# Kernel optimization log

Measured on AMD Instinct MI355X. Metric: run time of the kernel, lower is better.

## Reference

```python
import jax, jax.numpy as jnp
import numpy as np

VOCAB, D_EMB, H, M, B, L = 50000, 512, 512, 512, 1024, 64


def _lstm_last_h(x, seqlen, kernel, bias):
    """Run BasicLSTMCell over time; return hidden state at t=seqlen (TF dynamic_rnn semantics).
    x: [B, L, D], seqlen: [B], kernel: [D+H, 4H] (i,j,f,o), bias: [4H]."""
    Bc, Lc, _ = x.shape
    xT = jnp.swapaxes(x, 0, 1)  # [L, B, D]

    def step(carry, inp):
        c, h = carry
        xt, t = inp
        gates = jnp.concatenate([xt, h], axis=-1) @ kernel + bias
        i, j, f, o = jnp.split(gates, 4, axis=-1)
        new_c = c * jax.nn.sigmoid(f + 1.0) + jax.nn.sigmoid(i) * jnp.tanh(j)
        new_h = jnp.tanh(new_c) * jax.nn.sigmoid(o)
        mask = (t < seqlen)[:, None]
        return (jnp.where(mask, new_c, c), jnp.where(mask, new_h, h)), None

    z = jnp.zeros((Bc, kernel.shape[1] // 4), x.dtype)
    (c, h), _ = jax.lax.scan(step, (z, z), (xT, jnp.arange(Lc)))
    return h


def _reverse_seq(x, seqlen):
    """tf.reverse_sequence: reverse first seqlen steps per row, keep padding in place."""
    Bc, Lc, _ = x.shape
    t = jnp.arange(Lc)[None, :]
    idx = jnp.where(t < seqlen[:, None], seqlen[:, None] - 1 - t, t)
    return jnp.take_along_axis(x, idx[:, :, None], axis=1)


def _encode(x, seqlen, k_fw, b_fw, k_bw, b_bw):
    h_fw = _lstm_last_h(x, seqlen, k_fw, b_fw)
    h_bw = _lstm_last_h(_reverse_seq(x, seqlen), seqlen, k_bw, b_bw)
    return jnp.concatenate([h_fw, h_bw], axis=1)  # [B, 2H]


def setup_inputs() -> dict:
    key = jax.random.key(0)
    ks = jax.random.split(key, 12)
    s_emb = 1.0 / np.sqrt(D_EMB)
    s_k = 1.0 / np.sqrt(D_EMB + H)
    return {
        "input1": jax.random.randint(ks[0], (B, L), 0, VOCAB, dtype=jnp.int32),
        "input2": jax.random.randint(ks[1], (B, L), 0, VOCAB, dtype=jnp.int32),
        "seqlen1": jax.random.randint(ks[2], (B,), 1, L + 1, dtype=jnp.int32),
        "seqlen2": jax.random.randint(ks[3], (B,), 1, L + 1, dtype=jnp.int32),
        "embedding": jax.random.normal(ks[4], (VOCAB, D_EMB), jnp.float32) * s_emb,
        "k_fw": jax.random.normal(ks[5], (D_EMB + H, 4 * H), jnp.float32) * s_k,
        "b_fw": jnp.zeros((4 * H,), jnp.float32),
        "k_bw": jax.random.normal(ks[6], (D_EMB + H, 4 * H), jnp.float32) * s_k,
        "b_bw": jnp.zeros((4 * H,), jnp.float32),
        "W1": jax.random.normal(ks[7], (3 * 2 * H + 1, M), jnp.float32) / np.sqrt(6 * H + 1),
        "b1": jax.random.normal(ks[8], (1, M), jnp.float32) * 0.01,
        "W2": jax.random.normal(ks[9], (M, 2), jnp.float32) / np.sqrt(M),
        "b2": jax.random.normal(ks[10], (1, 2), jnp.float32) * 0.01,
    }


def reference(input1, input2, seqlen1, seqlen2, embedding, k_fw, b_fw, k_bw, b_bw, W1, b1, W2, b2):
    x1 = embedding[input1]  # [B, L, D]
    x2 = embedding[input2]
    h1 = _encode(x1, seqlen1, k_fw, b_fw, k_bw, b_bw)  # [B, 2H]
    h2 = _encode(x2, seqlen2, k_fw, b_fw, k_bw, b_bw)
    h_dist = jnp.sum(jnp.square(h1 - h2), axis=1, keepdims=True)  # [B, 1]
    h_combined = jnp.concatenate([h1, h2, h_dist, h1 * h2], axis=1)  # [B, 6H+1]
    e1 = jax.nn.relu(h_combined @ W1 + b1)  # dropout keep_prob=1 at inference
    preds = e1 @ W2 + b2  # [B, 2]
    return preds
```

## Files before the change

kernel.cpp:

```cpp
#include <hip/hip_runtime.h>
#include <hip/hip_bf16.h>
#include <cstddef>

#define VOCAB 50000
#define D_EMB 512
#define HDIM  512
#define MDIM  512
#define BATCH 1024
#define SEQL  64
#define ROWS  2048
#define KTOT  1024
#define HC_K  3136

typedef _Float16 f16;
typedef __attribute__((ext_vector_type(8))) _Float16 f16x8;
typedef __attribute__((ext_vector_type(4))) float f32x4;

__device__ __forceinline__ float sigf(float x) {
    return 1.0f / (1.0f + __expf(-x));
}
__device__ __forceinline__ float tanh_fast(float x) {
    x = fminf(30.0f, fmaxf(-30.0f, x));
    float t = __expf(-2.0f * x);
    return (1.0f - t) / (1.0f + t);
}
__device__ __forceinline__ void glds16(const void* g, const void* lds) {
    __builtin_amdgcn_global_load_lds(
        (const __attribute__((address_space(1))) unsigned int*)g,
        (__attribute__((address_space(3))) unsigned int*)lds, 16, 0, 0);
}

__global__ __launch_bounds__(256) void conv_emb(const float* __restrict__ src,
                                                f16* __restrict__ dst, int n8) {
    int i = blockIdx.x * 256 + threadIdx.x;
    if (i >= n8) return;
    const float4* s = (const float4*)src + (size_t)i * 2;
    float4 a = s[0], b = s[1];
    f16x8 o = {(f16)a.x, (f16)a.y, (f16)a.z, (f16)a.w,
               (f16)b.x, (f16)b.y, (f16)b.z, (f16)b.w};
    *(f16x8*)&dst[(size_t)i * 8] = o;
}

__global__ __launch_bounds__(256) void pack_w(const float* __restrict__ kfw,
                                              const float* __restrict__ kbw,
                                              f16* __restrict__ Wt) {
    unsigned idx = blockIdx.x * 256 + threadIdx.x;
    int k    = idx & 1023;
    int colp = (idx >> 10) & 2047;
    int d    = idx >> 21;
    int cg = colp >> 6, g = (colp >> 4) & 3, ci = colp & 15;
    int n = cg * 16 + ci;
    const float* K = d ? kbw : kfw;
    Wt[idx] = (f16)K[(size_t)k * 2048 + g * 512 + n];
}

__global__ __launch_bounds__(256) void pack_w1(const float* __restrict__ W1,
                                               f16* __restrict__ W1t) {
    int idx = blockIdx.x * 256 + threadIdx.x;
    if (idx >= 512 * HC_K) return;
    int k = idx % HC_K, c = idx / HC_K;
    W1t[idx] = (k < 3073) ? (f16)W1[(size_t)k * MDIM + c] : (f16)0.0f;
}

__global__ __launch_bounds__(256, 2) void lstm_step(
    int t,
    const int* __restrict__ in1, const int* __restrict__ in2,
    const int* __restrict__ sl1, const int* __restrict__ sl2,
    const f16* __restrict__ embH,
    const f16* __restrict__ Wt,
    const float* __restrict__ bfw, const float* __restrict__ bbw,
    const f16* __restrict__ hin,
    f16* __restrict__ hout,
    float* __restrict__ cbuf)
{
    const int dir = blockIdx.z;
    const int bx  = blockIdx.x;
    const int by  = blockIdx.y;
    const int tid = threadIdx.x;
    const int l = tid & 63, w = tid >> 6;

    __shared__ f16 Atile[2][128 * 64];
    __shared__ f16 Btile[2][128 * 64];
    __shared__ int toks[128];
    __shared__ int slens[128];

    if (tid < 128) {
        int r = by * 128 + tid;
        int b = r & (BATCH - 1);
        const int* inp = (r < BATCH) ? in1 : in2;
        int s = (r < BATCH) ? sl1[b] : sl2[b];
        int tt = t;
        if (dir == 1) tt = (t < s) ? (s - 1 - t) : t;
        toks[tid]  = inp[b * SEQL + tt];
        slens[tid] = s;
    }
    __syncthreads();

    const int kg8 = (((l & 7) ^ ((l >> 3) & 7))) * 8;
    int aoffX[4]; int hoff[4]; size_t boff[4]; int dst[4];
#pragma unroll
    for (int r = 0; r < 4; ++r) {
        int row = r * 32 + w * 8 + (l >> 3);
        aoffX[r] = toks[row] * 512 + kg8;
        hoff[r]  = ((dir * ROWS + by * 128 + row) << 9) + kg8;
        boff[r]  = ((size_t)(dir * 2048 + bx * 128 + row) << 10) + kg8;
        dst[r]   = (r * 32 + w * 8) * 64;
    }

    f32x4 acc[4][4];
#pragma unroll
    for (int i = 0; i < 4; ++i)
#pragma unroll
        for (int j = 0; j < 4; ++j) acc[i][j] = (f32x4){0.f, 0.f, 0.f, 0.f};

    const int wr = w >> 1, wc = w & 1;

#pragma unroll
    for (int r = 0; r < 4; ++r) {
        glds16(embH + aoffX[r], &Atile[0][dst[r]]);
        glds16(Wt + boff[r], &Btile[0][dst[r]]);
    }
    __syncthreads();

    int cur = 0;
    for (int kt = 0; kt < 16; ++kt) {
        if (kt < 15) {
            const int kn = kt + 1;
#pragma unroll
            for (int r = 0; r < 4; ++r) {
                const f16* asrc = (kn < 8) ? (embH + aoffX[r] + kn * 64)
                                           : (hin + hoff[r] + (kn - 8) * 64);
                glds16(asrc, &Atile[cur ^ 1][dst[r]]);
                glds16(Wt + boff[r] + kn * 64, &Btile[cur ^ 1][dst[r]]);
            }
        }
#pragma unroll
        for (int kk = 0; kk < 2; ++kk) {
            f16x8 af[4], bv[4];
            const int slot = (l >> 4) + kk * 4;
#pragma unroll
            for (int fm = 0; fm < 4; ++fm) {
                int row = wr * 64 + fm * 16 + (l & 15);
                af[fm] = *(const f16x8*)&Atile[cur][row * 64 + (slot ^ (row & 7)) * 8];
            }
#pragma unroll
            for (int fn = 0; fn < 4; ++fn) {
                int col = wc * 64 + fn * 16 + (l & 15);
                bv[fn] = *(const f16x8*)&Btile[cur][col * 64 + (slot ^ (col & 7)) * 8];
            }
#pragma unroll
            for (int fm = 0; fm < 4; ++fm)
#pragma unroll
                for (int fn = 0; fn < 4; ++fn)
                    acc[fm][fn] = __builtin_amdgcn_mfma_f32_16x16x32_f16(
                        af[fm], bv[fn], acc[fm][fn], 0, 0, 0);
        }
        __syncthreads();
        cur ^= 1;
    }

    const float* bias = dir ? bbw : bfw;
    const int cell = bx * 32 + wc * 16 + (l & 15);
    float bg[4];
#pragma unroll
    for (int g = 0; g < 4; ++g) bg[g] = bias[g * 512 + cell];

#pragma unroll
    for (int fm = 0; fm < 4; ++fm) {
#pragma unroll
        for (int reg = 0; reg < 4; ++reg) {
            int rl = wr * 64 + fm * 16 + (l >> 4) * 4 + reg;
            bool act = (t < slens[rl]);
            size_t idx = ((size_t)(dir * ROWS + by * 128 + rl) << 9) + cell;
            float gi = acc[fm][0][reg] + bg[0];
            float gj = acc[fm][1][reg] + bg[1];
            float gf = acc[fm][2][reg] + bg[2];
            float go = acc[fm][3][reg] + bg[3];
            if (act) {
                float cold = cbuf[idx];
                float cn = cold * sigf(gf + 1.0f) + sigf(gi) * tanh_fast(gj);
                float hn = tanh_fast(cn) * sigf(go);
                cbuf[idx] = cn;
                hout[idx] = (f16)hn;
            } else {
                hout[idx] = hin[idx];
            }
        }
    }
}

__global__ __launch_bounds__(256) void build_hc(const f16* __restrict__ hfin,
                                                f16* __restrict__ hc) {
    int b = blockIdx.x;
    int tid = threadIdx.x;
    __shared__ float red[256];
    float d = 0.0f;
    size_t base = (size_t)b * HC_K;
    for (int k = tid; k < 1024; k += 256) {
        int dir = k >> 9, kk = k & 511;
        size_t i1 = ((size_t)(dir * ROWS + b) << 9) + kk;
        size_t i2 = ((size_t)(dir * ROWS + BATCH + b) << 9) + kk;
        float h1 = (float)hfin[i1];
        float h2 = (float)hfin[i2];
        hc[base + k]        = (f16)h1;
        hc[base + 1024 + k] = (f16)h2;
        hc[base + 2049 + k] = (f16)(h1 * h2);
        float df = h1 - h2;
        d += df * df;
    }
    red[tid] = d;
    __syncthreads();
    for (int s = 128; s > 0; s >>= 1) {
        if (tid < s) red[tid] += red[tid + s];
        __syncthreads();
    }
    if (tid == 0) hc[base + 2048] = (f16)red[0];
    if (tid < HC_K - 3073) hc[base + 3073 + tid] = (f16)0.0f;
}

__global__ __launch_bounds__(256) void mlp1(const f16* __restrict__ hc,
                                            const f16* __restrict__ W1t,
                                            const float* __restrict__ b1,
                                            float* __restrict__ e1) {
    const int bx = blockIdx.x, by = blockIdx.y, tid = threadIdx.x;
    const int l = tid & 63, w = tid >> 6;
    __shared__ f16 Atile[2][64 * 64];
    __shared__ f16 Btile[2][64 * 64];

    const int kg8 = (((l & 7) ^ ((l >> 3) & 7))) * 8;
    size_t aoff[2], boff[2]; int dst[2];
#pragma unroll
    for (int g = 0; g < 2; ++g) {
        int row = g * 32 + w * 8 + (l >> 3);
        aoff[g] = (size_t)(by * 64 + row) * HC_K + kg8;
        boff[g] = (size_t)(bx * 64 + row) * HC_K + kg8;
        dst[g]  = (g * 32 + w * 8) * 64;
    }

    f32x4 acc[2][2];
#pragma unroll
    for (int i = 0; i < 2; ++i)
#pragma unroll
        for (int j = 0; j < 2; ++j) acc[i][j] = (f32x4){0.f, 0.f, 0.f, 0.f};

    const int wr = w >> 1, wc = w & 1;

#pragma unroll
    for (int g = 0; g < 2; ++g) {
        glds16(hc + aoff[g], &Atile[0][dst[g]]);
        glds16(W1t + boff[g], &Btile[0][dst[g]]);
    }
    __syncthreads();

    int cur = 0;
    for (int kt = 0; kt < HC_K / 64; ++kt) {
        if (kt < HC_K / 64 - 1) {
            const int kn = (kt + 1) * 64;
#pragma unroll
            for (int g = 0; g < 2; ++g) {
                glds16(hc + aoff[g] + kn, &Atile[cur ^ 1][dst[g]]);
                glds16(W1t + boff[g] + kn, &Btile[cur ^ 1][dst[g]]);
            }
        }
#pragma unroll
        for (int kk = 0; kk < 2; ++kk) {
            f16x8 af[2], bv[2];
            const int slot = (l >> 4) + kk * 4;
#pragma unroll
            for (int fm = 0; fm < 2; ++fm) {
                int row = wr * 32 + fm * 16 + (l & 15);
                af[fm] = *(const f16x8*)&Atile[cur][row * 64 + (slot ^ (row & 7)) * 8];
            }
#pragma unroll
            for (int fn = 0; fn < 2; ++fn) {
                int col = wc * 32 + fn * 16 + (l & 15);
                bv[fn] = *(const f16x8*)&Btile[cur][col * 64 + (slot ^ (col & 7)) * 8];
            }
#pragma unroll
            for (int fm = 0; fm < 2; ++fm)
#pragma unroll
                for (int fn = 0; fn < 2; ++fn)
                    acc[fm][fn] = __builtin_amdgcn_mfma_f32_16x16x32_f16(
                        af[fm], bv[fn], acc[fm][fn], 0, 0, 0);
        }
        __syncthreads();
        cur ^= 1;
    }

#pragma unroll
    for (int fm = 0; fm < 2; ++fm) {
#pragma unroll
        for (int fn = 0; fn < 2; ++fn) {
#pragma unroll
            for (int reg = 0; reg < 4; ++reg) {
                int r = by * 64 + wr * 32 + fm * 16 + (l >> 4) * 4 + reg;
                int c = bx * 64 + wc * 32 + fn * 16 + (l & 15);
                float v = acc[fm][fn][reg] + b1[c];
                e1[(size_t)r * MDIM + c] = v > 0.0f ? v : 0.0f;
            }
        }
    }
}

__global__ __launch_bounds__(64) void mlp2(const float* __restrict__ e1,
                                           const float* __restrict__ W2,
                                           const float* __restrict__ b2,
                                           float* __restrict__ out) {
    int b = blockIdx.x, tid = threadIdx.x;
    float p0 = 0.f, p1 = 0.f;
    for (int k = tid; k < 512; k += 64) {
        float e = e1[(size_t)b * MDIM + k];
        p0 += e * W2[2 * k];
        p1 += e * W2[2 * k + 1];
    }
    for (int off = 32; off > 0; off >>= 1) {
        p0 += __shfl_down(p0, off);
        p1 += __shfl_down(p1, off);
    }
    if (tid == 0) {
        out[2 * b]     = p0 + b2[0];
        out[2 * b + 1] = p1 + b2[1];
    }
}

extern "C" void kernel_launch(void* const* d_in, const int* in_sizes, int n_in,
                              void* d_out, int out_size, void* d_ws, size_t ws_size,
                              hipStream_t stream) {
    (void)in_sizes; (void)n_in; (void)out_size; (void)ws_size;
    const int*   in1 = (const int*)d_in[0];
    const int*   in2 = (const int*)d_in[1];
    const int*   sl1 = (const int*)d_in[2];
    const int*   sl2 = (const int*)d_in[3];
    const float* emb = (const float*)d_in[4];
    const float* kfw = (const float*)d_in[5];
    const float* bfw = (const float*)d_in[6];
    const float* kbw = (const float*)d_in[7];
    const float* bbw = (const float*)d_in[8];
    const float* W1  = (const float*)d_in[9];
    const float* b1  = (const float*)d_in[10];
    const float* W2  = (const float*)d_in[11];
    const float* b2  = (const float*)d_in[12];
    float* out = (float*)d_out;

    char* base = (char*)d_ws;
    f16*   embH = (f16*)base;
    f16*   Wt   = (f16*)(base + 51200000);
    f16*   W1t  = (f16*)(base + 59588608);
    float* cbuf = (float*)(base + 62799872);
    f16*   h0   = (f16*)(base + 71188480);
    f16*   h1   = (f16*)(base + 75382784);
    f16*   hc   = (f16*)(base + 79577088);
    float* e1   = (float*)(base + 85999616);

    hipMemsetAsync(cbuf, 0, 8388608, stream);
    hipMemsetAsync(h0, 0, 4194304, stream);

    conv_emb<<<(VOCAB * D_EMB / 8 + 255) / 256, 256, 0, stream>>>(emb, embH, VOCAB * D_EMB / 8);
    pack_w<<<(2 * 2048 * KTOT) / 256, 256, 0, stream>>>(kfw, kbw, Wt);
    pack_w1<<<(512 * HC_K + 255) / 256, 256, 0, stream>>>(W1, W1t);

    for (int t = 0; t < SEQL; ++t) {
        const f16* hi = (t & 1) ? h1 : h0;
        f16*       ho = (t & 1) ? h0 : h1;
        lstm_step<<<dim3(16, 16, 2), 256, 0, stream>>>(
            t, in1, in2, sl1, sl2, embH, Wt, bfw, bbw, hi, ho, cbuf);
    }

    build_hc<<<BATCH, 256, 0, stream>>>(h0, hc);
    mlp1<<<dim3(MDIM / 64, BATCH / 64), 256, 0, stream>>>(hc, W1t, b1, e1);
    mlp2<<<BATCH, 64, 0, stream>>>(e1, W2, b2, out);
}
```

Baseline: 2.081 ms.

## Sort rows by sequence length and skip finished row tiles in LSTM steps

Adds a kernel that ranks all 2048 rows by descending sequence length, producing a permutation, its inverse, and per-step active-row counts. Each LSTM step processes rows in permuted order and exits early for 128-row tiles where no row is still active, so later timesteps launch less work. The copy of h for inactive rows is dropped. The final hidden state is read from whichever ping-pong buffer matches each row's sequence-length parity, via the inverse permutation. The cost is an O(N^2) rank computation and gathered, non-contiguous row access in the step kernel.

New measurement: 1.985 ms. -4.6%, faster.

```diff
diff --git a/kernel.cpp b/kernel.cpp
--- a/kernel.cpp
+++ b/kernel.cpp
@@ -62,10 +62,39 @@
     W1t[idx] = (k < 3073) ? (f16)W1[(size_t)k * MDIM + c] : (f16)0.0f;
 }
 
+__global__ __launch_bounds__(256) void sort_rows(const int* __restrict__ sl1,
+                                                 const int* __restrict__ sl2,
+                                                 int* __restrict__ perm,
+                                                 int* __restrict__ inv,
+                                                 int* __restrict__ Acnt) {
+    __shared__ int s_sh[ROWS];
+    int tid = threadIdx.x;
+    for (int i = tid; i < ROWS; i += 256) {
+        int b = i & (BATCH - 1);
+        s_sh[i] = (i < BATCH) ? sl1[b] : sl2[b];
+    }
+    __syncthreads();
+    int i = blockIdx.x * 256 + tid;
+    int si = s_sh[i];
+    int rank = 0;
+    for (int j = 0; j < ROWS; ++j) {
+        int sj = s_sh[j];
+        rank += (sj > si) || (sj == si && j < i);
+    }
+    perm[rank] = i;
+    inv[i] = rank;
+    if (blockIdx.x == 0 && tid < SEQL) {
+        int c = 0;
+        for (int j = 0; j < ROWS; ++j) c += (s_sh[j] > tid);
+        Acnt[tid] = c;
+    }
+}
+
 __global__ __launch_bounds__(256, 2) void lstm_step(
     int t,
     const int* __restrict__ in1, const int* __restrict__ in2,
     const int* __restrict__ sl1, const int* __restrict__ sl2,
+    const int* __restrict__ perm, const int* __restrict__ Acnt,
     const f16* __restrict__ embH,
     const f16* __restrict__ Wt,
     const float* __restrict__ bfw, const float* __restrict__ bbw,
@@ -73,9 +102,10 @@
     f16* __restrict__ hout,
     float* __restrict__ cbuf)
 {
+    const int by  = blockIdx.y;
+    if (by * 128 >= Acnt[t]) return;
     const int dir = blockIdx.z;
     const int bx  = blockIdx.x;
-    const int by  = blockIdx.y;
     const int tid = threadIdx.x;
     const int l = tid & 63, w = tid >> 6;
 
@@ -85,7 +115,7 @@
     __shared__ int slens[128];
 
     if (tid < 128) {
-        int r = by * 128 + tid;
+        int r = perm[by * 128 + tid];
         int b = r & (BATCH - 1);
         const int* inp = (r < BATCH) ? in1 : in2;
         int s = (r < BATCH) ? sl1[b] : sl2[b];
@@ -170,38 +200,41 @@
 #pragma unroll
         for (int reg = 0; reg < 4; ++reg) {
             int rl = wr * 64 + fm * 16 + (l >> 4) * 4 + reg;
-            bool act = (t < slens[rl]);
-            size_t idx = ((size_t)(dir * ROWS + by * 128 + rl) << 9) + cell;
-            float gi = acc[fm][0][reg] + bg[0];
-            float gj = acc[fm][1][reg] + bg[1];
-            float gf = acc[fm][2][reg] + bg[2];
-            float go = acc[fm][3][reg] + bg[3];
-            if (act) {
+            if (t < slens[rl]) {
+                size_t idx = ((size_t)(dir * ROWS + by * 128 + rl) << 9) + cell;
+                float gi = acc[fm][0][reg] + bg[0];
+                float gj = acc[fm][1][reg] + bg[1];
+                float gf = acc[fm][2][reg] + bg[2];
+                float go = acc[fm][3][reg] + bg[3];
                 float cold = cbuf[idx];
                 float cn = cold * sigf(gf + 1.0f) + sigf(gi) * tanh_fast(gj);
                 float hn = tanh_fast(cn) * sigf(go);
                 cbuf[idx] = cn;
                 hout[idx] = (f16)hn;
-            } else {
-                hout[idx] = hin[idx];
-            }
-        }
-    }
-}
-
-__global__ __launch_bounds__(256) void build_hc(const f16* __restrict__ hfin,
+            }
+        }
+    }
+}
+
+__global__ __launch_bounds__(256) void build_hc(const f16* __restrict__ hbuf0,
+                                                const f16* __restrict__ hbuf1,
+                                                const int* __restrict__ sl1,
+                                                const int* __restrict__ sl2,
+                                                const int* __restrict__ inv,
                                                 f16* __restrict__ hc) {
     int b = blockIdx.x;
     int tid = threadIdx.x;
     __shared__ float red[256];
+    int s1 = sl1[b], s2 = sl2[b];
+    int p1 = inv[b], p2 = inv[BATCH + b];
+    const f16* hf1 = (s1 & 1) ? hbuf1 : hbuf0;
+    const f16* hf2 = (s2 & 1) ? hbuf1 : hbuf0;
     float d = 0.0f;
     size_t base = (size_t)b * HC_K;
     for (int k = tid; k < 1024; k += 256) {
         int dir = k >> 9, kk = k & 511;
-        size_t i1 = ((size_t)(dir * ROWS + b) << 9) + kk;
-        size_t i2 = ((size_t)(dir * ROWS + BATCH + b) << 9) + kk;
-        float h1 = (float)hfin[i1];
-        float h2 = (float)hfin[i2];
+        float h1 = (float)hf1[((size_t)(dir * ROWS + p1) << 9) + kk];
+        float h2 = (float)hf2[((size_t)(dir * ROWS + p2) << 9) + kk];
         hc[base + k]        = (f16)h1;
         hc[base + 1024 + k] = (f16)h2;
         hc[base + 2049 + k] = (f16)(h1 * h2);
@@ -351,10 +384,14 @@
     f16*   h1   = (f16*)(base + 75382784);
     f16*   hc   = (f16*)(base + 79577088);
     float* e1   = (float*)(base + 85999616);
+    int*   perm = (int*)(base + 88096768);
+    int*   inv  = (int*)(base + 88104960);
+    int*   Acnt = (int*)(base + 88113152);
 
     hipMemsetAsync(cbuf, 0, 8388608, stream);
     hipMemsetAsync(h0, 0, 4194304, stream);
 
+    sort_rows<<<ROWS / 256, 256, 0, stream>>>(sl1, sl2, perm, inv, Acnt);
     conv_emb<<<(VOCAB * D_EMB / 8 + 255) / 256, 256, 0, stream>>>(emb, embH, VOCAB * D_EMB / 8);
     pack_w<<<(2 * 2048 * KTOT) / 256, 256, 0, stream>>>(kfw, kbw, Wt);
     pack_w1<<<(512 * HC_K + 255) / 256, 256, 0, stream>>>(W1, W1t);
@@ -363,10 +400,10 @@
         const f16* hi = (t & 1) ? h1 : h0;
         f16*       ho = (t & 1) ? h0 : h1;
         lstm_step<<<dim3(16, 16, 2), 256, 0, stream>>>(
-            t, in1, in2, sl1, sl2, embH, Wt, bfw, bbw, hi, ho, cbuf);
-    }
-
-    build_hc<<<BATCH, 256, 0, stream>>>(h0, hc);
+            t, in1, in2, sl1, sl2, perm, Acnt, embH, Wt, bfw, bbw, hi, ho, cbuf);
+    }
+
+    build_hc<<<BATCH, 256, 0, stream>>>(h0, h1, sl1, sl2, inv, hc);
     mlp1<<<dim3(MDIM / 64, BATCH / 64), 256, 0, stream>>>(hc, W1t, b1, e1);
     mlp2<<<BATCH, 64, 0, stream>>>(e1, W2, b2, out);
 }
```
